# Performance work log

Measured on AMD Instinct MI355X. Metric: run time of the kernel, lower is better.

The kernel has to match this reference:

```python
import jax, jax.numpy as jnp
import numpy as np

SMOOTH = 1e-6
K = 64  # num_selection_features


def setup_inputs() -> dict:
    key = jax.random.key(0)
    kx, kw, kb = jax.random.split(key, 3)
    x = jax.random.normal(kx, (8, 256, 128, 128), dtype=jnp.float32)
    # 1x1 conv: Conv2d(K, 1) -> weight [1, K, 1, 1]; store as [K] and scalar bias
    w = jax.random.normal(kw, (K,), dtype=jnp.float32) * (1.0 / np.sqrt(K))
    b = jax.random.normal(kb, (1,), dtype=jnp.float32) * 0.01
    return {"x": x, "w": w, "b": b}


def reference(x, w, b):
    B, C, H, W = x.shape
    s = jax.nn.sigmoid(x)
    uncertainty = -s * jnp.log(s + SMOOTH)           # [B,C,H,W]
    score = jnp.mean(uncertainty, axis=(2, 3))       # [B,C]
    # topk smallest -> top_k of negated score
    _, idx = jax.lax.top_k(-score, K)                # [B,K]
    selected = jnp.take_along_axis(x, idx[:, :, None, None], axis=1)  # [B,K,H,W]
    # 1x1 conv (K->1) + sigmoid
    attn = jax.nn.sigmoid(jnp.einsum('bkhw,k->bhw', selected, w) + b[0])  # [B,H,W]
    return x * attn[:, None, :, :]
```

## Files before the change

kernel.cpp:

```cpp
#include <hip/hip_runtime.h>

constexpr int B  = 8;
constexpr int C  = 256;
constexpr int HW = 128 * 128;
constexpr int K  = 64;
#define SMOOTH 1e-6f

__device__ __forceinline__ float uncert(float v) {
    float s = 1.0f / (1.0f + expf(-v));
    return -s * logf(s + SMOOTH);
}

__global__ void score_kernel(const float* __restrict__ x, float* __restrict__ score) {
    const int plane = blockIdx.x;
    const float4* xp = (const float4*)(x + (size_t)plane * HW);
    const int t = threadIdx.x;

    float acc = 0.0f;
#pragma unroll
    for (int i = 0; i < 16; ++i) {
        float4 v = xp[t + i * 256];
        acc += uncert(v.x) + uncert(v.y) + uncert(v.z) + uncert(v.w);
    }
#pragma unroll
    for (int off = 32; off > 0; off >>= 1) acc += __shfl_down(acc, off, 64);

    __shared__ float smem[4];
    if ((t & 63) == 0) smem[t >> 6] = acc;
    __syncthreads();
    if (t == 0) score[plane] = (smem[0] + smem[1] + smem[2] + smem[3]) * (1.0f / HW);
}

__global__ void topk_kernel(const float* __restrict__ score, int* __restrict__ sel) {
    const int b = blockIdx.x;
    const int t = threadIdx.x;
    __shared__ float sc[C];
    sc[t] = score[b * C + t];
    __syncthreads();

    const float my = sc[t];
    int rank = 0;
#pragma unroll 8
    for (int j = 0; j < C; ++j) {
        float o = sc[j];
        rank += (o < my) || (o == my && j < t);
    }
    if (rank < K) sel[b * K + rank] = t;
}

__global__ void attn_kernel(const float* __restrict__ x, const int* __restrict__ sel,
                            const float* __restrict__ w, const float* __restrict__ bias,
                            float* __restrict__ attn) {
    const int b     = blockIdx.x >> 4;
    const int chunk = blockIdx.x & 15;
    const int t     = threadIdx.x;

    __shared__ float ws[K];
    __shared__ int   chs[K];
    if (t < K) { ws[t] = w[t]; chs[t] = sel[b * K + t]; }
    __syncthreads();

    const int p4 = chunk * 256 + t;
    const float4* xb = (const float4*)(x + (size_t)b * C * HW);

    float ax = 0.f, ay = 0.f, az = 0.f, aw = 0.f;
#pragma unroll 8
    for (int k = 0; k < K; ++k) {
        float4 v = xb[(size_t)chs[k] * (HW / 4) + p4];
        float wk = ws[k];
        ax += wk * v.x; ay += wk * v.y; az += wk * v.z; aw += wk * v.w;
    }
    const float b0 = bias[0];
    float4 o;
    o.x = 1.0f / (1.0f + expf(-(ax + b0)));
    o.y = 1.0f / (1.0f + expf(-(ay + b0)));
    o.z = 1.0f / (1.0f + expf(-(az + b0)));
    o.w = 1.0f / (1.0f + expf(-(aw + b0)));
    ((float4*)attn)[((size_t)b << 12) + p4] = o;
}

__global__ void mul_kernel(const float* __restrict__ x, const float* __restrict__ attn,
                           float* __restrict__ out) {
    const size_t i = (size_t)blockIdx.x * blockDim.x + threadIdx.x;
    const float4* x4 = (const float4*)x;
    const float4* a4 = (const float4*)attn;
    float4 v = x4[i];
    float4 a = a4[((i >> 20) << 12) | (i & 4095)];
    float4 o; o.x = v.x * a.x; o.y = v.y * a.y; o.z = v.z * a.z; o.w = v.w * a.w;
    ((float4*)out)[i] = o;
}

extern "C" void kernel_launch(void* const* d_in, const int* in_sizes, int n_in,
                              void* d_out, int out_size, void* d_ws, size_t ws_size,
                              hipStream_t stream) {
    const float* x    = (const float*)d_in[0];
    const float* w    = (const float*)d_in[1];
    const float* bias = (const float*)d_in[2];
    float* out = (float*)d_out;

    char* ws = (char*)d_ws;
    float* score = (float*)ws;
    int*   sel   = (int*)(ws + 8192);
    float* attn  = (float*)(ws + 16384);

    score_kernel<<<B * C, 256, 0, stream>>>(x, score);
    topk_kernel<<<B, C, 0, stream>>>(score, sel);
    attn_kernel<<<B * 16, 256, 0, stream>>>(x, sel, w, bias, attn);
    const int n4 = B * C * HW / 4;
    mul_kernel<<<n4 / 256, 256, 0, stream>>>(x, attn, out);
}
```

Before: 270.0 us.

## Fuse attention and multiply kernels, simplify uncertainty score with fast intrinsics

Merges the attention-map kernel and the broadcast multiply into one kernel, so each block computes the sigmoid attention for its pixels and then scales all 256 channels directly. This drops the attn buffer round-trip and one launch. The uncertainty score is rewritten with an algebraically rank-equivalent form (log2(1+e^-v)/(1+e^-v)), drops the SMOOTH term and the mean scaling, and uses fast exp/log/rcp intrinsics. Dropping SMOOTH and using approximate intrinsics can change near-tie orderings in top-k. The fused kernel launches only 256 blocks, each looping over 256 channels with float2 accesses, which may limit parallelism and memory throughput.

Result: no change. 270.5 us (+0.2%).

```diff
diff --git a/kernel.cpp b/kernel.cpp
--- a/kernel.cpp
+++ b/kernel.cpp
@@ -4,14 +4,15 @@
 constexpr int C  = 256;
 constexpr int HW = 128 * 128;
 constexpr int K  = 64;
-#define SMOOTH 1e-6f
 
-__device__ __forceinline__ float uncert(float v) {
-    float s = 1.0f / (1.0f + expf(-v));
-    return -s * logf(s + SMOOTH);
+__device__ __forceinline__ float uncert_rank(float v) {
+    float t = __expf(-v);
+    float a = 1.0f + t;
+    return __log2f(a) * __builtin_amdgcn_rcpf(a);
 }
 
-__global__ void score_kernel(const float* __restrict__ x, float* __restrict__ score) {
+__global__ __launch_bounds__(256) void score_kernel(const float* __restrict__ x,
+                                                    float* __restrict__ score) {
     const int plane = blockIdx.x;
     const float4* xp = (const float4*)(x + (size_t)plane * HW);
     const int t = threadIdx.x;
@@ -20,7 +21,7 @@
 #pragma unroll
     for (int i = 0; i < 16; ++i) {
         float4 v = xp[t + i * 256];
-        acc += uncert(v.x) + uncert(v.y) + uncert(v.z) + uncert(v.w);
+        acc += uncert_rank(v.x) + uncert_rank(v.y) + uncert_rank(v.z) + uncert_rank(v.w);
     }
 #pragma unroll
     for (int off = 32; off > 0; off >>= 1) acc += __shfl_down(acc, off, 64);
@@ -28,10 +29,11 @@
     __shared__ float smem[4];
     if ((t & 63) == 0) smem[t >> 6] = acc;
     __syncthreads();
-    if (t == 0) score[plane] = (smem[0] + smem[1] + smem[2] + smem[3]) * (1.0f / HW);
+    if (t == 0) score[plane] = smem[0] + smem[1] + smem[2] + smem[3];
 }
 
-__global__ void topk_kernel(const float* __restrict__ score, int* __restrict__ sel) {
+__global__ __launch_bounds__(256) void topk_kernel(const float* __restrict__ score,
+                                                   int* __restrict__ sel) {
     const int b = blockIdx.x;
     const int t = threadIdx.x;
     __shared__ float sc[C];
@@ -48,11 +50,13 @@
     if (rank < K) sel[b * K + rank] = t;
 }
 
-__global__ void attn_kernel(const float* __restrict__ x, const int* __restrict__ sel,
-                            const float* __restrict__ w, const float* __restrict__ bias,
-                            float* __restrict__ attn) {
-    const int b     = blockIdx.x >> 4;
-    const int chunk = blockIdx.x & 15;
+__global__ __launch_bounds__(256) void attn_mul_kernel(const float* __restrict__ x,
+                                                       const int* __restrict__ sel,
+                                                       const float* __restrict__ w,
+                                                       const float* __restrict__ bias,
+                                                       float* __restrict__ out) {
+    const int b     = blockIdx.x >> 5;
+    const int chunk = blockIdx.x & 31;
     const int t     = threadIdx.x;
 
     __shared__ float ws[K];
@@ -60,34 +64,30 @@
     if (t < K) { ws[t] = w[t]; chs[t] = sel[b * K + t]; }
     __syncthreads();
 
-    const int p4 = chunk * 256 + t;
-    const float4* xb = (const float4*)(x + (size_t)b * C * HW);
+    const int p2 = chunk * 256 + t;
+    const float2* xb = (const float2*)(x + (size_t)b * C * HW);
+    float2*       ob = (float2*)(out + (size_t)b * C * HW);
 
-    float ax = 0.f, ay = 0.f, az = 0.f, aw = 0.f;
-#pragma unroll 8
+    float ax = 0.f, ay = 0.f;
+#pragma unroll 16
     for (int k = 0; k < K; ++k) {
-        float4 v = xb[(size_t)chs[k] * (HW / 4) + p4];
+        float2 v = xb[(size_t)chs[k] * (HW / 2) + p2];
         float wk = ws[k];
-        ax += wk * v.x; ay += wk * v.y; az += wk * v.z; aw += wk * v.w;
+        ax += wk * v.x; ay += wk * v.y;
     }
     const float b0 = bias[0];
-    float4 o;
-    o.x = 1.0f / (1.0f + expf(-(ax + b0)));
-    o.y = 1.0f / (1.0f + expf(-(ay + b0)));
-    o.z = 1.0f / (1.0f + expf(-(az + b0)));
-    o.w = 1.0f / (1.0f + expf(-(aw + b0)));
-    ((float4*)attn)[((size_t)b << 12) + p4] = o;
-}
+    float ea = __expf(-(ax + b0));
+    float eb = __expf(-(ay + b0));
+    const float sa = __builtin_amdgcn_rcpf(1.0f + ea);
+    const float sb = __builtin_amdgcn_rcpf(1.0f + eb);
 
-__global__ void mul_kernel(const float* __restrict__ x, const float* __restrict__ attn,
-                           float* __restrict__ out) {
-    const size_t i = (size_t)blockIdx.x * blockDim.x + threadIdx.x;
-    const float4* x4 = (const float4*)x;
-    const float4* a4 = (const float4*)attn;
-    float4 v = x4[i];
-    float4 a = a4[((i >> 20) << 12) | (i & 4095)];
-    float4 o; o.x = v.x * a.x; o.y = v.y * a.y; o.z = v.z * a.z; o.w = v.w * a.w;
-    ((float4*)out)[i] = o;
+#pragma unroll 8
+    for (int c = 0; c < C; ++c) {
+        const size_t idx = (size_t)c * (HW / 2) + p2;
+        float2 v = xb[idx];
+        float2 o; o.x = v.x * sa; o.y = v.y * sb;
+        ob[idx] = o;
+    }
 }
 
 extern "C" void kernel_launch(void* const* d_in, const int* in_sizes, int n_in,
@@ -101,11 +101,8 @@
     char* ws = (char*)d_ws;
     float* score = (float*)ws;
     int*   sel   = (int*)(ws + 8192);
-    float* attn  = (float*)(ws + 16384);
 
     score_kernel<<<B * C, 256, 0, stream>>>(x, score);
     topk_kernel<<<B, C, 0, stream>>>(score, sel);
-    attn_kernel<<<B * 16, 256, 0, stream>>>(x, sel, w, bias, attn);
-    const int n4 = B * C * HW / 4;
-    mul_kernel<<<n4 / 256, 256, 0, stream>>>(x, attn, out);
+    attn_mul_kernel<<<B * 32, 256, 0, stream>>>(x, sel, w, bias, out);
 }
```
